# Optimization experiments

Hardware: AMD Instinct MI355X
Metric: run time of the kernel (lower is better)

Reference implementation:

```python
import jax, jax.numpy as jnp
import numpy as np

B, N, F = 8, 1024, 256
H, U = 4, 256
NEG = -1e9  # unused (adjacency=None -> full attention)


def setup_inputs() -> dict:
    key = jax.random.key(0)
    k1, k2, k3, k4 = jax.random.split(key, 4)
    x = jax.random.normal(k1, (B, N, F), dtype=jnp.float32)
    # glorot-scale params
    W = jax.random.normal(k2, (H, F, U), dtype=jnp.float32) * (2.0 / (F + U)) ** 0.5
    a_src = jax.random.normal(k3, (H, U, 1), dtype=jnp.float32) * (2.0 / (U + 1)) ** 0.5
    a_dst = jax.random.normal(k4, (H, U, 1), dtype=jnp.float32) * (2.0 / (U + 1)) ** 0.5
    return {"x": x, "W": W, "a_src": a_src, "a_dst": a_dst}


def reference(x, W, a_src, a_dst):
    # per-head linear projection: [B,H,N,U]
    h = jnp.einsum('bnf,hfu->bhnu', x, W)
    # additive attention logits
    src = jnp.einsum('bhnu,hu->bhn', h, a_src[..., 0])  # [B,H,N]
    dst = jnp.einsum('bhnu,hu->bhn', h, a_dst[..., 0])  # [B,H,N]
    scores = src[:, :, :, None] + dst[:, :, None, :]    # [B,H,N,N]
    scores = jax.nn.leaky_relu(scores, negative_slope=0.2)
    attn = jax.nn.softmax(scores, axis=-1)
    h_prime = jnp.einsum('bhnm,bhmu->bhnu', attn, h)    # [B,H,N,U]
    # concat heads: [B,N,H*U]
    return jnp.transpose(h_prime, (0, 2, 1, 3)).reshape(B, N, H * U)
```

## Files before the change

### kernel.cpp

```cpp
#include <hip/hip_runtime.h>
#include <math.h>

constexpr int B_ = 8, N_ = 1024, F_ = 256, H_ = 4, U_ = 256;
constexpr int BH_ = B_ * H_;
constexpr int CH_ = 16;
constexpr int NCH_ = N_ / CH_;
constexpr int M_ = B_ * N_;

typedef short short8 __attribute__((ext_vector_type(8)));
typedef float floatx4 __attribute__((ext_vector_type(4)));

__device__ inline unsigned short f2bf(float f) {
    unsigned u = __float_as_uint(f);
    u += 0x7fff + ((u >> 16) & 1);
    return (unsigned short)(u >> 16);
}
__device__ inline float bf2f(unsigned short s) { return __uint_as_float(((unsigned)s) << 16); }

__device__ inline void gload_lds16(const void* g, void* l) {
    __builtin_amdgcn_global_load_lds(
        (const __attribute__((address_space(1))) void*)g,
        (__attribute__((address_space(3))) void*)(unsigned)(uintptr_t)l,
        16, 0, 0);
}

__global__ __launch_bounds__(256) void prep_w(const float* __restrict__ W,
                                              const float* __restrict__ asr,
                                              const float* __restrict__ ads,
                                              unsigned short* __restrict__ whT,
                                              float* __restrict__ c_src,
                                              float* __restrict__ c_dst) {
    int tid = threadIdx.x;
    if (blockIdx.x < 64) {
        __shared__ float t[64][65];
        int bi = blockIdx.x;
        int f0 = (bi & 3) * 64, u0 = ((bi >> 2) & 3) * 64, h = bi >> 4;
        int c = tid & 63, rbase = tid >> 6;
        #pragma unroll
        for (int rr = 0; rr < 16; ++rr) {
            int r = rr * 4 + rbase;
            t[r][c] = W[((size_t)(h * F_ + f0 + r)) * U_ + u0 + c];
        }
        __syncthreads();
        #pragma unroll
        for (int rr = 0; rr < 16; ++rr) {
            int r = rr * 4 + rbase;
            whT[((size_t)(h * U_ + u0 + r)) * F_ + f0 + c] = f2bf(t[c][r]);
        }
    } else {
        int id = blockIdx.x - 64;
        int h = id >> 2, f0 = (id & 3) * 64;
        int fl = tid >> 2, q = tid & 3;
        int f = f0 + fl;
        const float* Wrow = W + ((size_t)(h * F_ + f)) * U_ + q * 64;
        const float* av = asr + h * U_ + q * 64;
        const float* bv = ads + h * U_ + q * 64;
        float s = 0.f, d = 0.f;
        #pragma unroll
        for (int u = 0; u < 64; ++u) { float ww = Wrow[u]; s += ww * av[u]; d += ww * bv[u]; }
        s += __shfl_xor(s, 1); s += __shfl_xor(s, 2);
        d += __shfl_xor(d, 1); d += __shfl_xor(d, 2);
        if (q == 0) { c_src[h * F_ + f] = s; c_dst[h * F_ + f] = d; }
    }
}

__global__ __launch_bounds__(256) void k1b_fused(const float* __restrict__ x,
                                                 const float* __restrict__ c_src,
                                                 const float* __restrict__ c_dst,
                                                 unsigned short* __restrict__ xh,
                                                 float* __restrict__ srcv,
                                                 float* __restrict__ dstv) {
    int tid = threadIdx.x;
    int lane = tid & 63, w = tid >> 6;
    int row = blockIdx.x * 4 + w;
    int b = row >> 10, n = row & 1023;
    const float4 x4 = *(const float4*)(x + (size_t)row * F_ + lane * 4);
    ushort4 hv;
    hv.x = f2bf(x4.x); hv.y = f2bf(x4.y); hv.z = f2bf(x4.z); hv.w = f2bf(x4.w);
    ((ushort4*)xh)[(size_t)row * (F_ / 4) + lane] = hv;
    #pragma unroll
    for (int hh = 0; hh < H_; ++hh) {
        float4 c4 = *(const float4*)(c_src + hh * F_ + lane * 4);
        float s = x4.x*c4.x + x4.y*c4.y + x4.z*c4.z + x4.w*c4.w;
        #pragma unroll
        for (int off = 32; off; off >>= 1) s += __shfl_xor(s, off);
        float4 d4 = *(const float4*)(c_dst + hh * F_ + lane * 4);
        float d = x4.x*d4.x + x4.y*d4.y + x4.z*d4.z + x4.w*d4.w;
        #pragma unroll
        for (int off = 32; off; off >>= 1) d += __shfl_xor(d, off);
        if (lane == 0) {
            srcv[(size_t)(b * H_ + hh) * N_ + n] = s;
            dstv[(size_t)(b * H_ + hh) * N_ + n] = d;
        }
    }
}

__device__ inline void bitonic1024(float& key, int& idx, float* keyL, int* idxL, int t) {
    for (int k = 2; k <= N_; k <<= 1) {
        for (int j = k >> 1; j > 0; j >>= 1) {
            bool up = ((t & k) == 0);
            bool lower = ((t & j) == 0);
            float ok; int od;
            if (j >= 64) {
                keyL[t] = key; idxL[t] = idx;
                __syncthreads();
                ok = keyL[t ^ j]; od = idxL[t ^ j];
                __syncthreads();
            } else {
                ok = __shfl_xor(key, j);
                od = __shfl_xor(idx, j);
            }
            bool sw = up ? (lower ? (key > ok) : (key < ok))
                         : (lower ? (key < ok) : (key > ok));
            if (sw) { key = ok; idx = od; }
        }
    }
}

__global__ __launch_bounds__(1024) void k2_all(const float* __restrict__ dstv,
                                               const float* __restrict__ srcv,
                                               float* __restrict__ dvs,
                                               int* __restrict__ invp,
                                               int* __restrict__ spos,
                                               int* __restrict__ srows,
                                               float* __restrict__ se8,
                                               int* __restrict__ cstart) {
    __shared__ float dv[N_];
    __shared__ float keyL[N_];
    __shared__ int   idxL[N_];
    int bh = blockIdx.x, t = threadIdx.x;

    float key = dstv[(size_t)bh * N_ + t]; int idx = t;
    bitonic1024(key, idx, keyL, idxL, t);
    dvs[(size_t)bh * N_ + t] = key;
    invp[(size_t)bh * N_ + idx] = t;
    dv[t] = key;

    float key2 = -srcv[(size_t)bh * N_ + t]; int idx2 = t;
    bitonic1024(key2, idx2, keyL, idxL, t);
    float s = -key2;
    float tt = key2;
    int lo = 0, hi = N_;
    while (lo < hi) {
        int mid = (lo + hi) >> 1;
        if (dv[mid] <= tt) lo = mid + 1; else hi = mid;
    }
    spos[(size_t)bh * N_ + t] = lo;
    srows[(size_t)bh * N_ + t] = idx2;
    se8[(size_t)bh * N_ + t] = expf(0.8f * s);
    __syncthreads();
    idxL[t] = lo;
    __syncthreads();
    if (t < NCH_ + 1) {
        int target = t * CH_;
        int lo2 = 0, hi2 = N_;
        while (lo2 < hi2) {
            int mid = (lo2 + hi2) >> 1;
            if (idxL[mid] < target) lo2 = mid + 1; else hi2 = mid;
        }
        cstart[bh * (NCH_ + 1) + t] = lo2;
    }
}

__global__ __launch_bounds__(256) void k1_mfma(const unsigned short* __restrict__ xh,
                                               const unsigned short* __restrict__ whT,
                                               const int* __restrict__ invp,
                                               unsigned short* __restrict__ hbuf) {
    __shared__ __align__(16) unsigned short As[128 * 64];
    __shared__ __align__(16) unsigned short Bs[128 * 64];
    const int tid = threadIdx.x;
    const int lane = tid & 63, wv = tid >> 6;
    const int wr = wv >> 1, wc = wv & 1;
    const int m0 = blockIdx.x * 128;
    const int u0 = blockIdx.y * 128;
    const int hh = blockIdx.z;

    floatx4 acc[4][4] = {};

    const char* Asrc = (const char*)xh;
    const char* Bsrc = (const char*)(whT + (size_t)hh * U_ * F_);

    const int ch_row = lane >> 3;
    const int ch_col = (lane & 7) * 16;

    for (int t = 0; t < 4; ++t) {
        const size_t kb = (size_t)t * 128;
        #pragma unroll
        for (int i = 0; i < 4; ++i) {
            int c = wv * 4 + i;
            int row = c * 8 + ch_row;
            gload_lds16(Asrc + (size_t)(m0 + row) * 512 + kb + ch_col,
                        (char*)As + c * 1024);
            gload_lds16(Bsrc + (size_t)(u0 + row) * 512 + kb + ch_col,
                        (char*)Bs + c * 1024);
        }
        __syncthreads();
        #pragma unroll
        for (int ks = 0; ks < 2; ++ks) {
            short8 af[4], bfr[4];
            #pragma unroll
            for (int mf = 0; mf < 4; ++mf) {
                int row = wr * 64 + mf * 16 + (lane & 15);
                af[mf] = *(const short8*)&As[row * 64 + ks * 32 + (lane >> 4) * 8];
            }
            #pragma unroll
            for (int nf = 0; nf < 4; ++nf) {
                int row = wc * 64 + nf * 16 + (lane & 15);
                bfr[nf] = *(const short8*)&Bs[row * 64 + ks * 32 + (lane >> 4) * 8];
            }
            #pragma unroll
            for (int mf = 0; mf < 4; ++mf)
                #pragma unroll
                for (int nf = 0; nf < 4; ++nf)
                    acc[mf][nf] = __builtin_amdgcn_mfma_f32_16x16x32_bf16(
                        af[mf], bfr[nf], acc[mf][nf], 0, 0, 0);
        }
        __syncthreads();
    }

    const int rquad = (lane >> 4) * 4;
    const int ucol = lane & 15;
    #pragma unroll
    for (int mf = 0; mf < 4; ++mf) {
        #pragma unroll
        for (int j = 0; j < 4; ++j) {
            int m = m0 + wr * 64 + mf * 16 + rquad + j;
            int b = m >> 10, n = m & 1023;
            int bh = b * H_ + hh;
            int js = invp[(size_t)bh * N_ + n];
            unsigned short* orow = hbuf + ((size_t)bh * N_ + js) * U_ + u0 + wc * 64;
            #pragma unroll
            for (int nf = 0; nf < 4; ++nf)
                orow[nf * 16 + ucol] = f2bf(acc[mf][nf][j]);
        }
    }
}

__global__ __launch_bounds__(256) void k3a_partial(const unsigned short* __restrict__ hbuf,
                                                   const float* __restrict__ dvs,
                                                   float* __restrict__ cT1, float* __restrict__ cT2,
                                                   float* __restrict__ cZ1, float* __restrict__ cZ2) {
    __shared__ float w1s[CH_], w2s[CH_];
    __shared__ floatx4 A1s[4][64], A2s[4][64];
    int bh = blockIdx.x / NCH_, c = blockIdx.x % NCH_;
    int tid = threadIdx.x, w = tid >> 6, l = tid & 63;
    const ushort4* hb4 = (const ushort4*)(hbuf + ((size_t)bh * N_ + c * CH_) * U_);
    ushort4 h0 = hb4[(4 * w + 0) * 64 + l];
    ushort4 h1 = hb4[(4 * w + 1) * 64 + l];
    ushort4 h2 = hb4[(4 * w + 2) * 64 + l];
    ushort4 h3 = hb4[(4 * w + 3) * 64 + l];
    floatx4 v0 = {bf2f(h0.x), bf2f(h0.y), bf2f(h0.z), bf2f(h0.w)};
    floatx4 v1 = {bf2f(h1.x), bf2f(h1.y), bf2f(h1.z), bf2f(h1.w)};
    floatx4 v2 = {bf2f(h2.x), bf2f(h2.y), bf2f(h2.z), bf2f(h2.w)};
    floatx4 v3 = {bf2f(h3.x), bf2f(h3.y), bf2f(h3.z), bf2f(h3.w)};
    if (tid < CH_) {
        float vv = dvs[(size_t)bh * N_ + c * CH_ + tid];
        w1s[tid] = expf(vv);
        w2s[tid] = expf(0.2f * vv);
    }
    __syncthreads();
    floatx4 s1 = w1s[4*w]*v0 + w1s[4*w+1]*v1 + w1s[4*w+2]*v2 + w1s[4*w+3]*v3;
    floatx4 s2 = w2s[4*w]*v0 + w2s[4*w+1]*v1 + w2s[4*w+2]*v2 + w2s[4*w+3]*v3;
    A1s[w][l] = s1; A2s[w][l] = s2;
    __syncthreads();
    if (tid < 64) {
        floatx4 r1 = A1s[0][tid] + A1s[1][tid] + A1s[2][tid] + A1s[3][tid];
        floatx4 r2 = A2s[0][tid] + A2s[1][tid] + A2s[2][tid] + A2s[3][tid];
        ((floatx4*)(cT1 + (size_t)(bh * NCH_ + c) * U_))[tid] = r1;
        ((floatx4*)(cT2 + (size_t)(bh * NCH_ + c) * U_))[tid] = r2;
    }
    if (tid == 0) {
        float z1 = 0.f, z2 = 0.f;
        #pragma unroll
        for (int r = 0; r < CH_; ++r) { z1 += w1s[r]; z2 += w2s[r]; }
        cZ1[bh * NCH_ + c] = z1; cZ2[bh * NCH_ + c] = z2;
    }
}

__global__ __launch_bounds__(256) void k3b_combine(const float* __restrict__ cT1, const float* __restrict__ cT2,
                                                   const float* __restrict__ cZ1, const float* __restrict__ cZ2,
                                                   float* __restrict__ b1, float* __restrict__ b2,
                                                   float* __restrict__ bz1, float* __restrict__ bz2) {
    int bh = blockIdx.x;
    int u = threadIdx.x;
    float v[NCH_];
    #pragma unroll
    for (int c = 0; c < NCH_; ++c) v[c] = cT2[(size_t)(bh * NCH_ + c) * U_ + u];
    float acc2 = 0.f;
    #pragma unroll
    for (int c = 0; c < NCH_; ++c) {
        b2[(size_t)(bh * NCH_ + c) * U_ + u] = acc2;
        acc2 += v[c];
    }
    #pragma unroll
    for (int c = 0; c < NCH_; ++c) v[c] = cT1[(size_t)(bh * NCH_ + c) * U_ + u];
    float acc1 = 0.f;
    #pragma unroll
    for (int c = NCH_ - 1; c >= 0; --c) {
        b1[(size_t)(bh * NCH_ + c) * U_ + u] = acc1;
        acc1 += v[c];
    }
    if (u < NCH_) {
        float z1 = cZ1[bh * NCH_ + u];
        float z2 = cZ2[bh * NCH_ + u];
        float i1 = z1, i2 = z2;
        #pragma unroll
        for (int off = 1; off < NCH_; off <<= 1) {
            float t1 = __shfl_up(i1, off, 64);
            float t2 = __shfl_up(i2, off, 64);
            if (u >= off) { i1 += t1; i2 += t2; }
        }
        float tot1 = __shfl(i1, NCH_ - 1, 64);
        bz1[bh * NCH_ + u] = tot1 - i1;
        bz2[bh * NCH_ + u] = i2 - z2;
    }
}

__global__ __launch_bounds__(256) void k3cd_emit(const unsigned short* __restrict__ hbuf,
                                                 const float* __restrict__ dvs,
                                                 const float* __restrict__ b1, const float* __restrict__ b2,
                                                 const float* __restrict__ bz1, const float* __restrict__ bz2,
                                                 const int* __restrict__ spos,
                                                 const int* __restrict__ srows,
                                                 const float* __restrict__ se8,
                                                 const int* __restrict__ cstart,
                                                 float* __restrict__ out) {
    __shared__ floatx4 P1s[CH_ + 1][64];
    __shared__ floatx4 P2s[CH_ + 1][64];
    __shared__ floatx4 T1s[4][64], T2s[4][64];
    __shared__ float w1s[CH_], w2s[CH_];
    __shared__ float zx1[CH_ + 1], zx2[CH_ + 1];
    __shared__ int sps[256], srs[256];
    __shared__ float s8s[256];

    int bh = blockIdx.x / NCH_, c = blockIdx.x % NCH_;
    int tid = threadIdx.x, w = tid >> 6, l = tid & 63;
    int b = bh >> 2, hh = bh & 3;

    const ushort4* hb4 = (const ushort4*)(hbuf + ((size_t)bh * N_ + c * CH_) * U_);
    ushort4 h0 = hb4[(4 * w + 0) * 64 + l];
    ushort4 h1 = hb4[(4 * w + 1) * 64 + l];
    ushort4 h2 = hb4[(4 * w + 2) * 64 + l];
    ushort4 h3 = hb4[(4 * w + 3) * 64 + l];
    floatx4 v0 = {bf2f(h0.x), bf2f(h0.y), bf2f(h0.z), bf2f(h0.w)};
    floatx4 v1 = {bf2f(h1.x), bf2f(h1.y), bf2f(h1.z), bf2f(h1.w)};
    floatx4 v2 = {bf2f(h2.x), bf2f(h2.y), bf2f(h2.z), bf2f(h2.w)};
    floatx4 v3 = {bf2f(h3.x), bf2f(h3.y), bf2f(h3.z), bf2f(h3.w)};
    if (tid < CH_) {
        float vv = dvs[(size_t)bh * N_ + c * CH_ + tid];
        w1s[tid] = expf(vv);
        w2s[tid] = expf(0.2f * vv);
    }
    __syncthreads();
    float a0 = w1s[4*w], a1 = w1s[4*w+1], a2 = w1s[4*w+2], a3 = w1s[4*w+3];
    float c0 = w2s[4*w], c1 = w2s[4*w+1], c2 = w2s[4*w+2], c3 = w2s[4*w+3];
    floatx4 q1_1 = a0 * v0;
    floatx4 q1_2 = q1_1 + a1 * v1;
    floatx4 q1_3 = q1_2 + a2 * v2;
    floatx4 tw1  = q1_3 + a3 * v3;
    floatx4 q2_1 = c0 * v0;
    floatx4 q2_2 = q2_1 + c1 * v1;
    floatx4 q2_3 = q2_2 + c2 * v2;
    floatx4 tw2  = q2_3 + c3 * v3;
    T1s[w][l] = tw1; T2s[w][l] = tw2;
    if (tid == 0) {
        float z1 = 0.f, z2 = 0.f;
        #pragma unroll
        for (int r = 0; r < CH_; ++r) { zx1[r] = z1; zx2[r] = z2; z1 += w1s[r]; z2 += w2s[r]; }
        zx1[CH_] = z1; zx2[CH_] = z2;
    }
    __syncthreads();
    floatx4 base1 = {0.f, 0.f, 0.f, 0.f}, base2 = {0.f, 0.f, 0.f, 0.f};
    if (w > 0) { base1 += T1s[0][l]; base2 += T2s[0][l]; }
    if (w > 1) { base1 += T1s[1][l]; base2 += T2s[1][l]; }
    if (w > 2) { base1 += T1s[2][l]; base2 += T2s[2][l]; }
    P1s[4*w+0][l] = base1;         P2s[4*w+0][l] = base2;
    P1s[4*w+1][l] = base1 + q1_1;  P2s[4*w+1][l] = base2 + q2_1;
    P1s[4*w+2][l] = base1 + q1_2;  P2s[4*w+2][l] = base2 + q2_2;
    P1s[4*w+3][l] = base1 + q1_3;  P2s[4*w+3][l] = base2 + q2_3;
    if (w == 3) { P1s[CH_][l] = base1 + tw1; P2s[CH_][l] = base2 + tw2; }
    __syncthreads();

    floatx4 t1 = P1s[CH_][l];
    float tz1 = zx1[CH_];
    floatx4 b1u = ((const floatx4*)(b1 + (size_t)(bh * NCH_ + c) * U_))[l];
    floatx4 b2u = ((const floatx4*)(b2 + (size_t)(bh * NCH_ + c) * U_))[l];
    float bz1c = bz1[bh * NCH_ + c], bz2c = bz2[bh * NCH_ + c];

    const int*   spos_b  = spos  + (size_t)bh * N_;
    const int*   srows_b = srows + (size_t)bh * N_;
    const float* se8_b   = se8   + (size_t)bh * N_;
    const int j0 = cstart[bh * (NCH_ + 1) + c];
    const int e0 = (c == NCH_ - 1) ? N_ : cstart[bh * (NCH_ + 1) + c + 1];

    for (int t0 = j0; t0 < e0; t0 += 256) {
        int jj = t0 + tid;
        if (jj < e0) { sps[tid] = spos_b[jj]; srs[tid] = srows_b[jj]; s8s[tid] = se8_b[jj]; }
        __syncthreads();
        int cnt = min(256, e0 - t0);
        for (int k = w; k < cnt; k += 4) {
            int   rr  = sps[k] - c * CH_;
            int   row = srs[k];
            float e8  = s8s[k];
            floatx4 s1 = b1u + (t1 - P1s[rr][l]);
            floatx4 s2 = b2u + P2s[rr][l];
            float den = e8 * (bz1c + (tz1 - zx1[rr])) + (bz2c + zx2[rr]);
            float rden = 1.0f / den;
            floatx4 o = (e8 * s1 + s2) * rden;
            *(floatx4*)(out + ((size_t)(b * N_ + row)) * (H_ * U_) + hh * U_ + 4 * l) = o;
        }
        __syncthreads();
    }
}

extern "C" void kernel_launch(void* const* d_in, const int* in_sizes, int n_in,
                              void* d_out, int out_size, void* d_ws, size_t ws_size,
                              hipStream_t stream) {
    const float* x    = (const float*)d_in[0];
    const float* W    = (const float*)d_in[1];
    const float* asr  = (const float*)d_in[2];
    const float* ads  = (const float*)d_in[3];
    float* out = (float*)d_out;

    char* ws = (char*)d_ws;
    size_t off = 0;
    auto alloc = [&](size_t nfloats) -> float* {
        float* p = (float*)(ws + off);
        off += ((nfloats * 4 + 255) / 256) * 256;
        return p;
    };
    unsigned short* hbuf = (unsigned short*)alloc((size_t)BH_ * N_ * U_ / 2);
    float* srcv  = alloc((size_t)BH_ * N_);
    float* dstv  = alloc((size_t)BH_ * N_);
    float* c_src = alloc(H_ * F_);
    float* c_dst = alloc(H_ * F_);
    float* dvs   = alloc((size_t)BH_ * N_);
    int*   invp  = (int*)alloc((size_t)BH_ * N_);
    int*   srows = (int*)alloc((size_t)BH_ * N_);
    int*   spos  = (int*)alloc((size_t)BH_ * N_);
    float* se8   = alloc((size_t)BH_ * N_);
    int*   cstart= (int*)alloc(BH_ * (NCH_ + 1));
    float* cT1   = alloc((size_t)BH_ * NCH_ * U_);
    float* cT2   = alloc((size_t)BH_ * NCH_ * U_);
    float* cZ1   = alloc(BH_ * NCH_);
    float* cZ2   = alloc(BH_ * NCH_);
    float* b1    = alloc((size_t)BH_ * NCH_ * U_);
    float* b2    = alloc((size_t)BH_ * NCH_ * U_);
    float* bz1   = alloc(BH_ * NCH_);
    float* bz2   = alloc(BH_ * NCH_);
    unsigned short* xh  = (unsigned short*)alloc((size_t)M_ * F_ / 2);
    unsigned short* whT = (unsigned short*)alloc((size_t)H_ * U_ * F_ / 2);
    (void)ws_size; (void)in_sizes; (void)n_in; (void)out_size;

    prep_w<<<80, 256, 0, stream>>>(W, asr, ads, whT, c_src, c_dst);
    k1b_fused<<<(B_ * N_) / 4, 256, 0, stream>>>(x, c_src, c_dst, xh, srcv, dstv);
    k2_all<<<BH_, 1024, 0, stream>>>(dstv, srcv, dvs, invp, spos, srows, se8, cstart);
    k1_mfma<<<dim3(M_ / 128, U_ / 128, H_), 256, 0, stream>>>(xh, whT, invp, hbuf);
    k3a_partial<<<BH_ * NCH_, 256, 0, stream>>>(hbuf, dvs, cT1, cT2, cZ1, cZ2);
    k3b_combine<<<BH_, 256, 0, stream>>>(cT1, cT2, cZ1, cZ2, b1, b2, bz1, bz2);
    k3cd_emit<<<BH_ * NCH_, 256, 0, stream>>>(hbuf, dvs, b1, b2, bz1, bz2,
                                              spos, srows, se8, cstart, out);
}
```

Baseline: 87.64 us.

## Fuse dual bitonic sorts and stage GEMM epilogue through LDS for vector scatter

The k2 kernel now sorts the dst and src keys in one interleaved bitonic network, so the two sorts share one set of barriers and their shuffles can overlap. The k1 GEMM epilogue now writes the bf16 tile into shared memory, loads the permutation indices once per block, and scatters each permuted row to global memory as 16-byte vector stores. Before, each lane did scalar 2-byte stores and its own invp lookup. The cost is more LDS in k2 and an extra staging pass with a barrier in k1.

```diff
diff --git a/kernel.cpp b/kernel.cpp
--- a/kernel.cpp
+++ b/kernel.cpp
@@ -95,28 +95,6 @@
     }
 }
 
-__device__ inline void bitonic1024(float& key, int& idx, float* keyL, int* idxL, int t) {
-    for (int k = 2; k <= N_; k <<= 1) {
-        for (int j = k >> 1; j > 0; j >>= 1) {
-            bool up = ((t & k) == 0);
-            bool lower = ((t & j) == 0);
-            float ok; int od;
-            if (j >= 64) {
-                keyL[t] = key; idxL[t] = idx;
-                __syncthreads();
-                ok = keyL[t ^ j]; od = idxL[t ^ j];
-                __syncthreads();
-            } else {
-                ok = __shfl_xor(key, j);
-                od = __shfl_xor(idx, j);
-            }
-            bool sw = up ? (lower ? (key > ok) : (key < ok))
-                         : (lower ? (key < ok) : (key > ok));
-            if (sw) { key = ok; idx = od; }
-        }
-    }
-}
-
 __global__ __launch_bounds__(1024) void k2_all(const float* __restrict__ dstv,
                                                const float* __restrict__ srcv,
                                                float* __restrict__ dvs,
@@ -126,37 +104,60 @@
                                                float* __restrict__ se8,
                                                int* __restrict__ cstart) {
     __shared__ float dv[N_];
-    __shared__ float keyL[N_];
-    __shared__ int   idxL[N_];
+    __shared__ float keyLA[N_]; __shared__ int idxLA[N_];
+    __shared__ float keyLB[N_]; __shared__ int idxLB[N_];
     int bh = blockIdx.x, t = threadIdx.x;
 
-    float key = dstv[(size_t)bh * N_ + t]; int idx = t;
-    bitonic1024(key, idx, keyL, idxL, t);
-    dvs[(size_t)bh * N_ + t] = key;
-    invp[(size_t)bh * N_ + idx] = t;
-    dv[t] = key;
-
-    float key2 = -srcv[(size_t)bh * N_ + t]; int idx2 = t;
-    bitonic1024(key2, idx2, keyL, idxL, t);
-    float s = -key2;
-    float tt = key2;
+    float ka = dstv[(size_t)bh * N_ + t];  int ia = t;
+    float kb = -srcv[(size_t)bh * N_ + t]; int ib = t;
+
+    for (int k = 2; k <= N_; k <<= 1) {
+        for (int j = k >> 1; j > 0; j >>= 1) {
+            bool up = ((t & k) == 0);
+            bool lower = ((t & j) == 0);
+            float oa, ob; int oia, oib;
+            if (j >= 64) {
+                keyLA[t] = ka; idxLA[t] = ia;
+                keyLB[t] = kb; idxLB[t] = ib;
+                __syncthreads();
+                oa = keyLA[t ^ j]; oia = idxLA[t ^ j];
+                ob = keyLB[t ^ j]; oib = idxLB[t ^ j];
+                __syncthreads();
+            } else {
+                oa = __shfl_xor(ka, j); oia = __shfl_xor(ia, j);
+                ob = __shfl_xor(kb, j); oib = __shfl_xor(ib, j);
+            }
+            bool swa = up ? (lower ? (ka > oa) : (ka < oa))
+                          : (lower ? (ka < oa) : (ka > oa));
+            if (swa) { ka = oa; ia = oia; }
+            bool swb = up ? (lower ? (kb > ob) : (kb < ob))
+                          : (lower ? (kb < ob) : (kb > ob));
+            if (swb) { kb = ob; ib = oib; }
+        }
+    }
+
+    dvs[(size_t)bh * N_ + t] = ka;
+    invp[(size_t)bh * N_ + ia] = t;
+    dv[t] = ka;
+    __syncthreads();
+
+    float s = -kb;
     int lo = 0, hi = N_;
     while (lo < hi) {
         int mid = (lo + hi) >> 1;
-        if (dv[mid] <= tt) lo = mid + 1; else hi = mid;
+        if (dv[mid] <= kb) lo = mid + 1; else hi = mid;
     }
     spos[(size_t)bh * N_ + t] = lo;
-    srows[(size_t)bh * N_ + t] = idx2;
+    srows[(size_t)bh * N_ + t] = ib;
     se8[(size_t)bh * N_ + t] = expf(0.8f * s);
-    __syncthreads();
-    idxL[t] = lo;
+    idxLA[t] = lo;
     __syncthreads();
     if (t < NCH_ + 1) {
         int target = t * CH_;
         int lo2 = 0, hi2 = N_;
         while (lo2 < hi2) {
             int mid = (lo2 + hi2) >> 1;
-            if (idxL[mid] < target) lo2 = mid + 1; else hi2 = mid;
+            if (idxLA[mid] < target) lo2 = mid + 1; else hi2 = mid;
         }
         cstart[bh * (NCH_ + 1) + t] = lo2;
     }
@@ -166,14 +167,17 @@
                                                const unsigned short* __restrict__ whT,
                                                const int* __restrict__ invp,
                                                unsigned short* __restrict__ hbuf) {
-    __shared__ __align__(16) unsigned short As[128 * 64];
-    __shared__ __align__(16) unsigned short Bs[128 * 64];
+    __shared__ __align__(16) unsigned short As[2 * 128 * 64];
+    __shared__ int jsL[128];
+    unsigned short* Bs = As + 128 * 64;
     const int tid = threadIdx.x;
     const int lane = tid & 63, wv = tid >> 6;
     const int wr = wv >> 1, wc = wv & 1;
     const int m0 = blockIdx.x * 128;
     const int u0 = blockIdx.y * 128;
     const int hh = blockIdx.z;
+    const int b = m0 >> 10, n0 = m0 & 1023;
+    const int bh = b * H_ + hh;
 
     floatx4 acc[4][4] = {};
 
@@ -218,21 +222,26 @@
         __syncthreads();
     }
 
+    unsigned short* S = As;
     const int rquad = (lane >> 4) * 4;
     const int ucol = lane & 15;
     #pragma unroll
-    for (int mf = 0; mf < 4; ++mf) {
+    for (int mf = 0; mf < 4; ++mf)
         #pragma unroll
         for (int j = 0; j < 4; ++j) {
-            int m = m0 + wr * 64 + mf * 16 + rquad + j;
-            int b = m >> 10, n = m & 1023;
-            int bh = b * H_ + hh;
-            int js = invp[(size_t)bh * N_ + n];
-            unsigned short* orow = hbuf + ((size_t)bh * N_ + js) * U_ + u0 + wc * 64;
+            int rloc = wr * 64 + mf * 16 + rquad + j;
             #pragma unroll
             for (int nf = 0; nf < 4; ++nf)
-                orow[nf * 16 + ucol] = f2bf(acc[mf][nf][j]);
-        }
+                S[rloc * 128 + wc * 64 + nf * 16 + ucol] = f2bf(acc[mf][nf][j]);
+        }
+    if (tid < 128) jsL[tid] = invp[(size_t)bh * N_ + n0 + tid];
+    __syncthreads();
+    #pragma unroll
+    for (int i = 0; i < 8; ++i) {
+        int flat = tid + i * 256;
+        int rloc = flat >> 4, slot = flat & 15;
+        short8 v = *(const short8*)&S[rloc * 128 + slot * 8];
+        *(short8*)&hbuf[((size_t)bh * N_ + jsL[rloc]) * U_ + u0 + slot * 8] = v;
     }
 }
 
```

Result: faster. 82.71 us (-5.6%).
